# Performance work log

Measured on AMD Instinct MI355X. Metric: run time of the kernel, lower is better.

## Reference

```python
import jax, jax.numpy as jnp
import numpy as np

B, S, H = 4, 1024, 2048
E = 16            # num_experts
K = 2             # num_experts_per_token
I = 1024          # per-expert intermediate_dim
N_SHARED = 2
I_SHARED = I * N_SHARED
RATIO = 0.1       # shared_expert_ratio
EPS = 1e-9


def _swiglu(x, wg, wu, wd):
    # SwiGLU, bias=False: down( silu(gate(x)) * up(x) )
    return (jax.nn.silu(x @ wg) * (x @ wu)) @ wd


def setup_inputs() -> dict:
    key = jax.random.key(0)
    ks = jax.random.split(key, 9)
    scale = 0.02
    x = jax.random.normal(ks[0], (B, S, H), dtype=jnp.float32)
    centroids = jax.random.normal(ks[1], (E, H), dtype=jnp.float32)  # nn.Parameter(randn)
    gate_bias = jnp.zeros((E,), dtype=jnp.float32)
    # shared expert SwiGLU weights (intermediate = I * n_shared_experts)
    wg_s = jax.random.normal(ks[2], (H, I_SHARED), dtype=jnp.float32) * scale
    wu_s = jax.random.normal(ks[3], (H, I_SHARED), dtype=jnp.float32) * scale
    wd_s = jax.random.normal(ks[4], (I_SHARED, H), dtype=jnp.float32) * scale
    # routed experts, stacked [E, ...]
    wg = jax.random.normal(ks[5], (E, H, I), dtype=jnp.float32) * scale
    wu = jax.random.normal(ks[6], (E, H, I), dtype=jnp.float32) * scale
    wd = jax.random.normal(ks[7], (E, I, H), dtype=jnp.float32) * scale
    return {"x": x, "centroids": centroids, "gate_bias": gate_bias,
            "wg_s": wg_s, "wu_s": wu_s, "wd_s": wd_s,
            "wg": wg, "wu": wu, "wd": wd}


def reference(x, centroids, gate_bias, wg_s, wu_s, wd_s, wg, wu, wd):
    # 1) shared expert on ALL tokens, scaled by ratio
    shared = _swiglu(x, wg_s, wu_s, wd_s) * RATIO          # [B,S,H]
    # 2) centroid affinity (DeepSeek-V3 sigmoid gating)
    affinity = jax.nn.sigmoid(jnp.einsum('bsh,eh->bse', x, centroids))  # [B,S,E]
    # 3) bias used ONLY for selection
    biased = affinity + gate_bias
    _, top_idx = jax.lax.top_k(biased, K)                  # [B,S,K]
    # 4) clean weights from unbiased affinity, normalized to sum 1
    top_aff = jnp.take_along_axis(affinity, top_idx, axis=-1)  # [B,S,K]
    weights = top_aff / (top_aff.sum(-1, keepdims=True) + EPS)
    # 5) combine-mask: per-token per-expert weight (0 if not selected)
    mask = (jax.nn.one_hot(top_idx, E, dtype=x.dtype) * weights[..., None]).sum(-2)  # [B,S,E]
    # 6) expert compute + weighted combine; loop over fixed small E avoids
    #    materializing a [B,S,E,H] tensor
    routed = jnp.zeros_like(x)
    for e in range(E):
        routed = routed + mask[..., e:e + 1] * _swiglu(x, wg[e], wu[e], wd[e])
    return shared + routed
```

## Files before the change

kernel.cpp:

```cpp
#include <hip/hip_runtime.h>
#include <hip/hip_bf16.h>

typedef unsigned short u16;
typedef unsigned int u32;
typedef unsigned long long u64;
typedef __attribute__((ext_vector_type(8))) short short8;
typedef __attribute__((ext_vector_type(4))) float f32x4;

#define TOKENS 4096
#define HDIM 2048
#define NEXP 16
#define IDIM 1024
#define ISH 2048
#define MAXT128 80
#define MAXT256 48
#define NCHUNK 128

#define AS1(p) ((const __attribute__((address_space(1))) u32*)(p))
#define AS3(p) ((__attribute__((address_space(3))) u32*)(p))

__device__ __forceinline__ u16 f2b(float f) {
    u32 u = __float_as_uint(f);
    u32 r = u + 0x7fffu + ((u >> 16) & 1u);
    return (u16)(r >> 16);
}

__global__ __launch_bounds__(256) void convert_x_kernel(const float* __restrict__ x,
                                                        u16* __restrict__ xb) {
    size_t i = ((size_t)blockIdx.x * 256 + threadIdx.x) * 8;
    float4 a = *(const float4*)(x + i);
    float4 b = *(const float4*)(x + i + 4);
    u32 p0 = (u32)f2b(a.x) | ((u32)f2b(a.y) << 16);
    u32 p1 = (u32)f2b(a.z) | ((u32)f2b(a.w) << 16);
    u32 p2 = (u32)f2b(b.x) | ((u32)f2b(b.y) << 16);
    u32 p3 = (u32)f2b(b.z) | ((u32)f2b(b.w) << 16);
    uint4 o = make_uint4(p0, p1, p2, p3);
    *(uint4*)(xb + i) = o;
}

__global__ __launch_bounds__(256) void route_kernel(const float* __restrict__ x,
                                                    const float* __restrict__ cent,
                                                    const float* __restrict__ bias,
                                                    int* __restrict__ top_e,
                                                    float* __restrict__ top_w) {
    __shared__ alignas(16) float cs[8 * 2048];
    int lane = threadIdx.x & 63;
    int wv = threadIdx.x >> 6;
    int t = blockIdx.x * 4 + wv;
    const float4* xp4 = (const float4*)(x + (size_t)t * HDIM);
    float4 xr[8];
#pragma unroll
    for (int i = 0; i < 8; i++) xr[i] = xp4[lane + 64 * i];
    float aff[16];
#pragma unroll
    for (int ph = 0; ph < 2; ph++) {
        if (ph) __syncthreads();
        const float* sbase = cent + (size_t)(ph * 8 + wv * 2) * HDIM;
        float* dbase = cs + (size_t)wv * 2 * HDIM;
#pragma unroll
        for (int i = 0; i < 16; i++) {
            __builtin_amdgcn_global_load_lds(AS1(sbase + i * 256 + lane * 4),
                                             AS3(dbase + i * 256), 16, 0, 0);
        }
        __syncthreads();
#pragma unroll
        for (int e = 0; e < 8; e++) {
            const float4* cp = (const float4*)cs + (size_t)e * 512;
            float s = 0.f;
#pragma unroll
            for (int i = 0; i < 8; i++) {
                float4 cv = cp[lane + 64 * i];
                s += xr[i].x * cv.x;
                s += xr[i].y * cv.y;
                s += xr[i].z * cv.z;
                s += xr[i].w * cv.w;
            }
#pragma unroll
            for (int off = 32; off > 0; off >>= 1) s += __shfl_xor(s, off, 64);
            aff[ph * 8 + e] = 1.f / (1.f + expf(-s));
        }
    }
    float b0 = -1e30f, b1 = -1e30f, a0 = 0.f, a1 = 0.f;
    int e0 = -1, e1 = -1;
#pragma unroll
    for (int e = 0; e < 16; e++) {
        float v = aff[e] + bias[e];
        if (v > b0) {
            b1 = b0; e1 = e0; a1 = a0;
            b0 = v; e0 = e; a0 = aff[e];
        } else if (v > b1) {
            b1 = v; e1 = e; a1 = aff[e];
        }
    }
    float inv = 1.f / (a0 + a1 + 1e-9f);
    if (lane == 0) {
        top_e[2 * t] = e0; top_w[2 * t] = a0 * inv;
        top_e[2 * t + 1] = e1; top_w[2 * t + 1] = a1 * inv;
    }
}

__global__ __launch_bounds__(1024) void build_kernel(
    const int* __restrict__ top_e, const float* __restrict__ top_w,
    int* __restrict__ counts, int* __restrict__ offsets,
    int* __restrict__ ntilesA, int* __restrict__ tileA_e, int* __restrict__ tileA_m,
    int* __restrict__ ntilesB, int* __restrict__ tileB_e, int* __restrict__ tileB_m,
    int* __restrict__ list_tok, float* __restrict__ list_w,
    int* __restrict__ tok2slot) {
    __shared__ int cnt[NCHUNK][16];
    __shared__ int offs_s[16];
    __shared__ int totals[16];
    int tid = threadIdx.x;
    int lane = tid & 63, wv = tid >> 6;
    for (int c = wv; c < NCHUNK; c += 16) {
        int v = top_e[c * 64 + lane];
#pragma unroll
        for (int e = 0; e < 16; e++) {
            u64 m = __ballot(v == e);
            if (lane == 0) cnt[c][e] = (int)__popcll(m);
        }
    }
    __syncthreads();
    if (tid < 16) {
        int s = 0;
        for (int c = 0; c < NCHUNK; c++) s += cnt[c][tid];
        totals[tid] = s;
        counts[tid] = s;
    }
    __syncthreads();
    if (tid == 0) {
        int r = 0, ntA = 0, ntB = 0;
        for (int e = 0; e < 16; e++) {
            offs_s[e] = r;
            offsets[e] = r;
            int ce = totals[e];
            int tA = (ce + 127) >> 7;
            for (int m = 0; m < tA; m++) { tileA_e[ntA] = e; tileA_m[ntA] = m; ntA++; }
            int tB = (ce + 255) >> 8;
            for (int m = 0; m < tB; m++) { tileB_e[ntB] = e; tileB_m[ntB] = m; ntB++; }
            r += ce;
        }
        *ntilesA = ntA;
        *ntilesB = ntB;
    }
    __syncthreads();
    if (tid < 16) {
        int r = offs_s[tid];
        for (int c = 0; c < NCHUNK; c++) {
            int v = cnt[c][tid];
            cnt[c][tid] = r;
            r += v;
        }
    }
    __syncthreads();
    for (int c = wv; c < NCHUNK; c += 16) {
        int i = c * 64 + lane;
        int v = top_e[i];
        int rank = 0;
#pragma unroll
        for (int e = 0; e < 16; e++) {
            u64 m = __ballot(v == e);
            if (v == e) rank = (int)__popcll(m & ((1ull << lane) - 1ull));
        }
        int slot = cnt[c][v] + rank;
        list_tok[slot] = i >> 1;
        list_w[slot] = top_w[i];
        tok2slot[i] = slot;
    }
}

__global__ __launch_bounds__(256) void conv_w_kernel(const float* __restrict__ W,
                                                     u16* __restrict__ Wt, int K, int N) {
    int nt = blockIdx.x, kc = blockIdx.y;
    size_t mato = (size_t)blockIdx.z * K * N;
    const float* Wm = W + mato;
    u16* Wtm = Wt + mato;
    int ksB = K >> 5;
    __shared__ u16 Ls[64 * 40];
    int t = threadIdx.x;
    int kr = t >> 3, ng = t & 7;
    int nn = t >> 2, seg = t & 3;
    int g = seg ^ ((nn >> 2) & 3);
#pragma unroll
    for (int s = 0; s < 8; s++) {
        int kb = kc * 256 + s * 32;
        const float* src = Wm + (size_t)(kb + kr) * N + nt * 64 + ng * 8;
        float4 f0 = *(const float4*)src;
        float4 f1 = *(const float4*)(src + 4);
        __syncthreads();
        const float* p0 = (const float*)&f0;
        const float* p1 = (const float*)&f1;
#pragma unroll
        for (int l = 0; l < 4; l++) Ls[(8 * ng + l) * 40 + kr] = f2b(p0[l]);
#pragma unroll
        for (int l = 0; l < 4; l++) Ls[(8 * ng + 4 + l) * 40 + kr] = f2b(p1[l]);
        __syncthreads();
        const u16* lp = &Ls[nn * 40 + g * 8];
        u32 w0 = (u32)lp[0] | ((u32)lp[1] << 16);
        u32 w1 = (u32)lp[2] | ((u32)lp[3] << 16);
        u32 w2 = (u32)lp[4] | ((u32)lp[5] << 16);
        u32 w3 = (u32)lp[6] | ((u32)lp[7] << 16);
        uint4 o = make_uint4(w0, w1, w2, w3);
        *(uint4*)(Wtm + (size_t)(nt * ksB + (kb >> 5)) * 2048 + t * 8) = o;
    }
}

__global__ __launch_bounds__(256) void gemm_gateup(
    const u16* __restrict__ A, const u16* __restrict__ BgAll, const u16* __restrict__ BuAll,
    u16* __restrict__ hout, int Kd, int Nout, const int* __restrict__ counts,
    const int* __restrict__ offsets, const int* __restrict__ ntiles,
    const int* __restrict__ tile_e, const int* __restrict__ tile_m,
    const int* __restrict__ list_tok, int routed) {
    int cnt = TOKENS, base = 0, m0;
    const u16* Bg = BgAll;
    const u16* Bu = BuAll;
    if (routed) {
        int ti = blockIdx.x;
        if (ti >= *ntiles) return;
        int e = tile_e[ti];
        m0 = tile_m[ti] * 128;
        cnt = counts[e];
        base = offsets[e];
        size_t off = (size_t)e * Kd * Nout;
        Bg += off; Bu += off;
    } else {
        m0 = blockIdx.x * 128;
    }
    int ksB = Kd >> 5;
    __shared__ alignas(16) u16 As[128 * 32];
    __shared__ alignas(16) u16 Bgs[64 * 32];
    __shared__ alignas(16) u16 Bus[64 * 32];
    int tid = threadIdx.x;
    int lane = tid & 63, wv = tid >> 6;
    int quad = lane >> 4, mr = lane & 15;
    int n0 = blockIdx.y * 64;
    int gk = (tid & 3) ^ ((tid >> 4) & 3);
    int mg0 = min(m0 + (tid >> 2), cnt - 1);
    int mg1 = min(m0 + 64 + (tid >> 2), cnt - 1);
    size_t sr0 = routed ? (size_t)list_tok[base + mg0] : (size_t)mg0;
    size_t sr1 = routed ? (size_t)list_tok[base + mg1] : (size_t)mg1;
    const u16* ap0 = A + sr0 * Kd + gk * 8;
    const u16* ap1 = A + sr1 * Kd + gk * 8;
    const u16* bgp = Bg + (size_t)blockIdx.y * ksB * 2048 + tid * 8;
    const u16* bup = Bu + (size_t)blockIdx.y * ksB * 2048 + tid * 8;
    u16* AsW = As + wv * 512;
    u16* AsW2 = As + 2048 + wv * 512;
    u16* BgsW = Bgs + wv * 512;
    u16* BusW = Bus + wv * 512;
    int xq = quad ^ ((mr >> 2) & 3);
    const short8* a0p = (const short8*)(As + ((32 * wv + mr) * 4 + xq) * 8);
    const short8* a1p = (const short8*)(As + ((32 * wv + 16 + mr) * 4 + xq) * 8);
    f32x4 accg[2][4], accu[2][4];
#pragma unroll
    for (int i = 0; i < 2; i++)
#pragma unroll
        for (int j = 0; j < 4; j++) { accg[i][j] = (f32x4)0.f; accu[i][j] = (f32x4)0.f; }

    for (int ks = 0; ks < ksB; ks++) {
        __syncthreads();
        __builtin_amdgcn_global_load_lds(AS1(ap0), AS3(AsW), 16, 0, 0);
        __builtin_amdgcn_global_load_lds(AS1(ap1), AS3(AsW2), 16, 0, 0);
        __builtin_amdgcn_global_load_lds(AS1(bgp), AS3(BgsW), 16, 0, 0);
        __builtin_amdgcn_global_load_lds(AS1(bup), AS3(BusW), 16, 0, 0);
        ap0 += 32; ap1 += 32; bgp += 2048; bup += 2048;
        __syncthreads();
        short8 a0 = *a0p;
        short8 a1 = *a1p;
#pragma unroll
        for (int j = 0; j < 4; j++) {
            short8 bg = *(const short8*)(Bgs + (64 * j + mr * 4 + xq) * 8);
            short8 bu = *(const short8*)(Bus + (64 * j + mr * 4 + xq) * 8);
            accg[0][j] = __builtin_amdgcn_mfma_f32_16x16x32_bf16(a0, bg, accg[0][j], 0, 0, 0);
            accg[1][j] = __builtin_amdgcn_mfma_f32_16x16x32_bf16(a1, bg, accg[1][j], 0, 0, 0);
            accu[0][j] = __builtin_amdgcn_mfma_f32_16x16x32_bf16(a0, bu, accu[0][j], 0, 0, 0);
            accu[1][j] = __builtin_amdgcn_mfma_f32_16x16x32_bf16(a1, bu, accu[1][j], 0, 0, 0);
        }
    }
#pragma unroll
    for (int i = 0; i < 2; i++)
#pragma unroll
        for (int j = 0; j < 4; j++)
#pragma unroll
            for (int r = 0; r < 4; r++) {
                int m = m0 + 32 * wv + 16 * i + quad * 4 + r;
                if (m < cnt) {
                    float gv = accg[i][j][r], uv = accu[i][j][r];
                    float h = gv / (1.f + expf(-gv)) * uv;
                    int n = n0 + 16 * j + mr;
                    hout[(size_t)(base + m) * Nout + n] = f2b(h);
                }
            }
}

__global__ __launch_bounds__(256) void gemm_down(
    const u16* __restrict__ A, const u16* __restrict__ BAll, float* __restrict__ outp,
    int Kd, const int* __restrict__ counts, const int* __restrict__ offsets,
    const int* __restrict__ ntiles, const int* __restrict__ tile_e,
    const int* __restrict__ tile_m, const int* __restrict__ list_tok, int routed) {
    int cnt = TOKENS, base = 0, m0;
    const u16* B = BAll;
    if (routed) {
        int ti = blockIdx.x;
        if (ti >= *ntiles) return;
        int e = tile_e[ti];
        m0 = tile_m[ti] * 256;
        cnt = counts[e];
        base = offsets[e];
        B += (size_t)e * Kd * HDIM;
    } else {
        m0 = blockIdx.x * 256;
    }
    int nk = Kd >> 5;
    __shared__ alignas(16) u16 As[2][256 * 32];
    __shared__ alignas(16) u16 Bs[2][64 * 32];
    int tid = threadIdx.x;
    int lane = tid & 63, wv = tid >> 6;
    int quad = lane >> 4, mr = lane & 15;
    int n0 = blockIdx.y * 64;
    int gk = (tid & 3) ^ ((tid >> 4) & 3);
    const u16* ap0;
    const u16* ap1;
    const u16* ap2;
    const u16* ap3;
    {
        int mg0 = base + min(m0 + 0 * 64 + (tid >> 2), cnt - 1);
        int mg1 = base + min(m0 + 1 * 64 + (tid >> 2), cnt - 1);
        int mg2 = base + min(m0 + 2 * 64 + (tid >> 2), cnt - 1);
        int mg3 = base + min(m0 + 3 * 64 + (tid >> 2), cnt - 1);
        ap0 = A + (size_t)mg0 * Kd + gk * 8;
        ap1 = A + (size_t)mg1 * Kd + gk * 8;
        ap2 = A + (size_t)mg2 * Kd + gk * 8;
        ap3 = A + (size_t)mg3 * Kd + gk * 8;
    }
    const u16* bp = B + (size_t)blockIdx.y * nk * 2048 + tid * 8;
    int xq = quad ^ ((mr >> 2) & 3);
    f32x4 acc[4][4];
#pragma unroll
    for (int i = 0; i < 4; i++)
#pragma unroll
        for (int j = 0; j < 4; j++) acc[i][j] = (f32x4)0.f;

#define STAGE_D(b)                                                                        \
    do {                                                                                  \
        __builtin_amdgcn_global_load_lds(AS1(ap0), AS3(&As[b][0 + wv * 512]), 16, 0, 0);  \
        __builtin_amdgcn_global_load_lds(AS1(ap1), AS3(&As[b][2048 + wv * 512]), 16, 0,   \
                                         0);                                              \
        __builtin_amdgcn_global_load_lds(AS1(ap2), AS3(&As[b][4096 + wv * 512]), 16, 0,   \
                                         0);                                              \
        __builtin_amdgcn_global_load_lds(AS1(ap3), AS3(&As[b][6144 + wv * 512]), 16, 0,   \
                                         0);                                              \
        __builtin_amdgcn_global_load_lds(AS1(bp), AS3(&Bs[b][wv * 512]), 16, 0, 0);       \
        ap0 += 32; ap1 += 32; ap2 += 32; ap3 += 32; bp += 2048;                           \
    } while (0)

    STAGE_D(0);
    __syncthreads();
    int cur = 0;
    for (int ks = 0; ks < nk; ks++) {
        if (ks + 1 < nk) STAGE_D(cur ^ 1);
        const u16* Asc = As[cur];
        const u16* Bc = Bs[cur];
        short8 a0 = *(const short8*)(Asc + ((64 * wv + 0 + mr) * 4 + xq) * 8);
        short8 a1 = *(const short8*)(Asc + ((64 * wv + 16 + mr) * 4 + xq) * 8);
        short8 a2 = *(const short8*)(Asc + ((64 * wv + 32 + mr) * 4 + xq) * 8);
        short8 a3 = *(const short8*)(Asc + ((64 * wv + 48 + mr) * 4 + xq) * 8);
#pragma unroll
        for (int j = 0; j < 4; j++) {
            short8 b = *(const short8*)(Bc + ((16 * j + mr) * 4 + xq) * 8);
            acc[0][j] = __builtin_amdgcn_mfma_f32_16x16x32_bf16(a0, b, acc[0][j], 0, 0, 0);
            acc[1][j] = __builtin_amdgcn_mfma_f32_16x16x32_bf16(a1, b, acc[1][j], 0, 0, 0);
            acc[2][j] = __builtin_amdgcn_mfma_f32_16x16x32_bf16(a2, b, acc[2][j], 0, 0, 0);
            acc[3][j] = __builtin_amdgcn_mfma_f32_16x16x32_bf16(a3, b, acc[3][j], 0, 0, 0);
        }
        __syncthreads();
        cur ^= 1;
    }
#undef STAGE_D

#pragma unroll
    for (int i = 0; i < 4; i++)
#pragma unroll
        for (int j = 0; j < 4; j++)
#pragma unroll
            for (int r = 0; r < 4; r++) {
                int m = m0 + 64 * wv + 16 * i + quad * 4 + r;
                if (m >= cnt) continue;
                int n = n0 + 16 * j + mr;
                float v = acc[i][j][r];
                if (routed) {
                    outp[(size_t)(base + m) * HDIM + n] = v;
                } else {
                    outp[(size_t)m * HDIM + n] = 0.1f * v;
                }
            }
}

__global__ __launch_bounds__(256) void combine_kernel(float* __restrict__ out,
                                                      const float* __restrict__ rd,
                                                      const int* __restrict__ tok2slot,
                                                      const float* __restrict__ top_w) {
    int t = blockIdx.x;
    int s0 = tok2slot[2 * t], s1 = tok2slot[2 * t + 1];
    float w0 = top_w[2 * t], w1 = top_w[2 * t + 1];
    const float4* r0 = (const float4*)(rd + (size_t)s0 * HDIM);
    const float4* r1 = (const float4*)(rd + (size_t)s1 * HDIM);
    float4* op = (float4*)(out + (size_t)t * HDIM);
#pragma unroll
    for (int k = 0; k < 2; k++) {
        int c = threadIdx.x + k * 256;
        float4 o = op[c];
        float4 a = r0[c];
        float4 b = r1[c];
        o.x += w0 * a.x + w1 * b.x;
        o.y += w0 * a.y + w1 * b.y;
        o.z += w0 * a.z + w1 * b.z;
        o.w += w0 * a.w + w1 * b.w;
        op[c] = o;
    }
}

extern "C" void kernel_launch(void* const* d_in, const int* in_sizes, int n_in,
                              void* d_out, int out_size, void* d_ws, size_t ws_size,
                              hipStream_t stream) {
    const float* x = (const float*)d_in[0];
    const float* cent = (const float*)d_in[1];
    const float* bias = (const float*)d_in[2];
    const float* wgs = (const float*)d_in[3];
    const float* wus = (const float*)d_in[4];
    const float* wds = (const float*)d_in[5];
    const float* wg = (const float*)d_in[6];
    const float* wu = (const float*)d_in[7];
    const float* wd = (const float*)d_in[8];
    float* out = (float*)d_out;
    char* ws = (char*)d_ws;

    size_t off_wtgs = 0;
    size_t off_wtus = off_wtgs + (size_t)HDIM * ISH * 2;
    size_t off_wtds = off_wtus + (size_t)HDIM * ISH * 2;
    size_t off_wtg = off_wtds + (size_t)ISH * HDIM * 2;
    size_t off_wtu = off_wtg + (size_t)NEXP * HDIM * IDIM * 2;
    size_t off_wtd = off_wtu + (size_t)NEXP * HDIM * IDIM * 2;
    size_t off_xbf = off_wtd + (size_t)NEXP * IDIM * HDIM * 2;
    size_t off_hsh = off_xbf + (size_t)TOKENS * HDIM * 2;
    size_t off_hrt = off_hsh + (size_t)TOKENS * ISH * 2;
    size_t off_meta = off_hrt + (size_t)2 * TOKENS * IDIM * 2;
    size_t need = off_meta + (1 << 20);
    if (ws_size < need) return;

    u16* Wt_gs = (u16*)(ws + off_wtgs);
    u16* Wt_us = (u16*)(ws + off_wtus);
    u16* Wt_ds = (u16*)(ws + off_wtds);
    u16* Wt_g = (u16*)(ws + off_wtg);
    u16* Wt_u = (u16*)(ws + off_wtu);
    u16* Wt_d = (u16*)(ws + off_wtd);
    u16* x_bf = (u16*)(ws + off_xbf);
    u16* h_sh = (u16*)(ws + off_hsh);
    u16* h_rt = (u16*)(ws + off_hrt);
    float* rd = (float*)ws;
    int* counts = (int*)(ws + off_meta);
    int* offsets = counts + 16;
    int* ntilesA = offsets + 16;
    int* ntilesB = ntilesA + 8;
    int* tileA_e = ntilesB + 8;
    int* tileA_m = tileA_e + MAXT128;
    int* tileB_e = tileA_m + MAXT128;
    int* tileB_m = tileB_e + MAXT256;
    int* tok2slot = tileB_m + MAXT256;
    int* top_e = tok2slot + 2 * TOKENS;
    float* top_w = (float*)(top_e + 2 * TOKENS);
    int* list_tok = (int*)(top_w + 2 * TOKENS);
    float* list_w = (float*)(list_tok + 2 * TOKENS);

    convert_x_kernel<<<TOKENS * HDIM / (256 * 8), 256, 0, stream>>>(x, x_bf);
    route_kernel<<<TOKENS / 4, 256, 0, stream>>>(x, cent, bias, top_e, top_w);
    build_kernel<<<1, 1024, 0, stream>>>(top_e, top_w, counts, offsets, ntilesA, tileA_e,
                                         tileA_m, ntilesB, tileB_e, tileB_m, list_tok,
                                         list_w, tok2slot);

    conv_w_kernel<<<dim3(ISH / 64, HDIM / 256, 1), 256, 0, stream>>>(wgs, Wt_gs, HDIM, ISH);
    conv_w_kernel<<<dim3(ISH / 64, HDIM / 256, 1), 256, 0, stream>>>(wus, Wt_us, HDIM, ISH);
    conv_w_kernel<<<dim3(HDIM / 64, ISH / 256, 1), 256, 0, stream>>>(wds, Wt_ds, ISH, HDIM);
    conv_w_kernel<<<dim3(IDIM / 64, HDIM / 256, NEXP), 256, 0, stream>>>(wg, Wt_g, HDIM, IDIM);
    conv_w_kernel<<<dim3(IDIM / 64, HDIM / 256, NEXP), 256, 0, stream>>>(wu, Wt_u, HDIM, IDIM);
    conv_w_kernel<<<dim3(HDIM / 64, IDIM / 256, NEXP), 256, 0, stream>>>(wd, Wt_d, IDIM, HDIM);

    gemm_gateup<<<dim3(TOKENS / 128, ISH / 64, 1), 256, 0, stream>>>(
        x_bf, Wt_gs, Wt_us, h_sh, HDIM, ISH, nullptr, nullptr, nullptr, nullptr, nullptr,
        nullptr, 0);
    gemm_down<<<dim3(TOKENS / 256, HDIM / 64, 1), 256, 0, stream>>>(
        h_sh, Wt_ds, out, ISH, nullptr, nullptr, nullptr, nullptr, nullptr, nullptr, 0);
    gemm_gateup<<<dim3(MAXT128, IDIM / 64, 1), 256, 0, stream>>>(
        x_bf, Wt_g, Wt_u, h_rt, HDIM, IDIM, counts, offsets, ntilesA, tileA_e, tileA_m,
        list_tok, 1);
    gemm_down<<<dim3(MAXT256, HDIM / 64, 1), 256, 0, stream>>>(
        h_rt, Wt_d, rd, IDIM, counts, offsets, ntilesB, tileB_e, tileB_m, list_tok, 1);
    combine_kernel<<<TOKENS, 256, 0, stream>>>(out, rd, tok2slot, top_w);
}
```

Measured before the change: 980.7 us.

## Double K-step per iteration in gate/up and down GEMMs, drop double buffering

Both GEMM kernels now load a K slice of 64 per iteration (two 32-wide sub-tiles) instead of 32, halving the number of barriers and loop iterations. The down GEMM removes its two-stage double-buffered prefetch in favor of a single larger buffer loaded synchronously each iteration. This trades fewer synchronizations and more loads in flight per barrier against losing the overlap of global loads with MFMA compute in the down kernel, and it uses more LDS in the gate/up kernel, which may reduce occupancy.

Result: faster. 884.0 us (-9.9%).

```diff
diff --git a/kernel.cpp b/kernel.cpp
--- a/kernel.cpp
+++ b/kernel.cpp
@@ -225,10 +225,10 @@
     } else {
         m0 = blockIdx.x * 128;
     }
-    int ksB = Kd >> 5;
-    __shared__ alignas(16) u16 As[128 * 32];
-    __shared__ alignas(16) u16 Bgs[64 * 32];
-    __shared__ alignas(16) u16 Bus[64 * 32];
+    int nk = Kd >> 6;
+    __shared__ alignas(16) u16 As[128 * 64];
+    __shared__ alignas(16) u16 Bgs[64 * 64];
+    __shared__ alignas(16) u16 Bus[64 * 64];
     int tid = threadIdx.x;
     int lane = tid & 63, wv = tid >> 6;
     int quad = lane >> 4, mr = lane & 15;
@@ -240,39 +240,41 @@
     size_t sr1 = routed ? (size_t)list_tok[base + mg1] : (size_t)mg1;
     const u16* ap0 = A + sr0 * Kd + gk * 8;
     const u16* ap1 = A + sr1 * Kd + gk * 8;
-    const u16* bgp = Bg + (size_t)blockIdx.y * ksB * 2048 + tid * 8;
-    const u16* bup = Bu + (size_t)blockIdx.y * ksB * 2048 + tid * 8;
-    u16* AsW = As + wv * 512;
-    u16* AsW2 = As + 2048 + wv * 512;
-    u16* BgsW = Bgs + wv * 512;
-    u16* BusW = Bus + wv * 512;
+    size_t bstr = (size_t)(Kd >> 5) * 2048;
+    const u16* bgp = Bg + (size_t)blockIdx.y * bstr + tid * 8;
+    const u16* bup = Bu + (size_t)blockIdx.y * bstr + tid * 8;
     int xq = quad ^ ((mr >> 2) & 3);
-    const short8* a0p = (const short8*)(As + ((32 * wv + mr) * 4 + xq) * 8);
-    const short8* a1p = (const short8*)(As + ((32 * wv + 16 + mr) * 4 + xq) * 8);
     f32x4 accg[2][4], accu[2][4];
 #pragma unroll
     for (int i = 0; i < 2; i++)
 #pragma unroll
         for (int j = 0; j < 4; j++) { accg[i][j] = (f32x4)0.f; accu[i][j] = (f32x4)0.f; }
 
-    for (int ks = 0; ks < ksB; ks++) {
-        __syncthreads();
-        __builtin_amdgcn_global_load_lds(AS1(ap0), AS3(AsW), 16, 0, 0);
-        __builtin_amdgcn_global_load_lds(AS1(ap1), AS3(AsW2), 16, 0, 0);
-        __builtin_amdgcn_global_load_lds(AS1(bgp), AS3(BgsW), 16, 0, 0);
-        __builtin_amdgcn_global_load_lds(AS1(bup), AS3(BusW), 16, 0, 0);
-        ap0 += 32; ap1 += 32; bgp += 2048; bup += 2048;
-        __syncthreads();
-        short8 a0 = *a0p;
-        short8 a1 = *a1p;
-#pragma unroll
-        for (int j = 0; j < 4; j++) {
-            short8 bg = *(const short8*)(Bgs + (64 * j + mr * 4 + xq) * 8);
-            short8 bu = *(const short8*)(Bus + (64 * j + mr * 4 + xq) * 8);
-            accg[0][j] = __builtin_amdgcn_mfma_f32_16x16x32_bf16(a0, bg, accg[0][j], 0, 0, 0);
-            accg[1][j] = __builtin_amdgcn_mfma_f32_16x16x32_bf16(a1, bg, accg[1][j], 0, 0, 0);
-            accu[0][j] = __builtin_amdgcn_mfma_f32_16x16x32_bf16(a0, bu, accu[0][j], 0, 0, 0);
-            accu[1][j] = __builtin_amdgcn_mfma_f32_16x16x32_bf16(a1, bu, accu[1][j], 0, 0, 0);
+    for (int ks = 0; ks < nk; ks++) {
+        __syncthreads();
+        __builtin_amdgcn_global_load_lds(AS1(ap0), AS3(As + wv * 512), 16, 0, 0);
+        __builtin_amdgcn_global_load_lds(AS1(ap0 + 32), AS3(As + 4096 + wv * 512), 16, 0, 0);
+        __builtin_amdgcn_global_load_lds(AS1(ap1), AS3(As + 2048 + wv * 512), 16, 0, 0);
+        __builtin_amdgcn_global_load_lds(AS1(ap1 + 32), AS3(As + 6144 + wv * 512), 16, 0, 0);
+        __builtin_amdgcn_global_load_lds(AS1(bgp), AS3(Bgs + wv * 512), 16, 0, 0);
+        __builtin_amdgcn_global_load_lds(AS1(bgp + 2048), AS3(Bgs + 2048 + wv * 512), 16, 0, 0);
+        __builtin_amdgcn_global_load_lds(AS1(bup), AS3(Bus + wv * 512), 16, 0, 0);
+        __builtin_amdgcn_global_load_lds(AS1(bup + 2048), AS3(Bus + 2048 + wv * 512), 16, 0, 0);
+        ap0 += 64; ap1 += 64; bgp += 4096; bup += 4096;
+        __syncthreads();
+#pragma unroll
+        for (int c = 0; c < 2; c++) {
+            short8 a0 = *(const short8*)(As + c * 4096 + ((32 * wv + mr) * 4 + xq) * 8);
+            short8 a1 = *(const short8*)(As + c * 4096 + ((32 * wv + 16 + mr) * 4 + xq) * 8);
+#pragma unroll
+            for (int j = 0; j < 4; j++) {
+                short8 bg = *(const short8*)(Bgs + c * 2048 + (64 * j + mr * 4 + xq) * 8);
+                short8 bu = *(const short8*)(Bus + c * 2048 + (64 * j + mr * 4 + xq) * 8);
+                accg[0][j] = __builtin_amdgcn_mfma_f32_16x16x32_bf16(a0, bg, accg[0][j], 0, 0, 0);
+                accg[1][j] = __builtin_amdgcn_mfma_f32_16x16x32_bf16(a1, bg, accg[1][j], 0, 0, 0);
+                accu[0][j] = __builtin_amdgcn_mfma_f32_16x16x32_bf16(a0, bu, accu[0][j], 0, 0, 0);
+                accu[1][j] = __builtin_amdgcn_mfma_f32_16x16x32_bf16(a1, bu, accu[1][j], 0, 0, 0);
+            }
         }
     }
 #pragma unroll
@@ -309,9 +311,9 @@
     } else {
         m0 = blockIdx.x * 256;
     }
-    int nk = Kd >> 5;
-    __shared__ alignas(16) u16 As[2][256 * 32];
-    __shared__ alignas(16) u16 Bs[2][64 * 32];
+    int nk = Kd >> 6;
+    __shared__ alignas(16) u16 As[256 * 64];
+    __shared__ alignas(16) u16 Bs[64 * 64];
     int tid = threadIdx.x;
     int lane = tid & 63, wv = tid >> 6;
     int quad = lane >> 4, mr = lane & 15;
@@ -331,7 +333,8 @@
         ap2 = A + (size_t)mg2 * Kd + gk * 8;
         ap3 = A + (size_t)mg3 * Kd + gk * 8;
     }
-    const u16* bp = B + (size_t)blockIdx.y * nk * 2048 + tid * 8;
+    size_t bstr = (size_t)(Kd >> 5) * 2048;
+    const u16* bp = B + (size_t)blockIdx.y * bstr + tid * 8;
     int xq = quad ^ ((mr >> 2) & 3);
     f32x4 acc[4][4];
 #pragma unroll
@@ -339,42 +342,36 @@
 #pragma unroll
         for (int j = 0; j < 4; j++) acc[i][j] = (f32x4)0.f;
 
-#define STAGE_D(b)                                                                        \
-    do {                                                                                  \
-        __builtin_amdgcn_global_load_lds(AS1(ap0), AS3(&As[b][0 + wv * 512]), 16, 0, 0);  \
-        __builtin_amdgcn_global_load_lds(AS1(ap1), AS3(&As[b][2048 + wv * 512]), 16, 0,   \
-                                         0);                                              \
-        __builtin_amdgcn_global_load_lds(AS1(ap2), AS3(&As[b][4096 + wv * 512]), 16, 0,   \
-                                         0);                                              \
-        __builtin_amdgcn_global_load_lds(AS1(ap3), AS3(&As[b][6144 + wv * 512]), 16, 0,   \
-                                         0);                                              \
-        __builtin_amdgcn_global_load_lds(AS1(bp), AS3(&Bs[b][wv * 512]), 16, 0, 0);       \
-        ap0 += 32; ap1 += 32; ap2 += 32; ap3 += 32; bp += 2048;                           \
-    } while (0)
-
-    STAGE_D(0);
-    __syncthreads();
-    int cur = 0;
     for (int ks = 0; ks < nk; ks++) {
-        if (ks + 1 < nk) STAGE_D(cur ^ 1);
-        const u16* Asc = As[cur];
-        const u16* Bc = Bs[cur];
-        short8 a0 = *(const short8*)(Asc + ((64 * wv + 0 + mr) * 4 + xq) * 8);
-        short8 a1 = *(const short8*)(Asc + ((64 * wv + 16 + mr) * 4 + xq) * 8);
-        short8 a2 = *(const short8*)(Asc + ((64 * wv + 32 + mr) * 4 + xq) * 8);
-        short8 a3 = *(const short8*)(Asc + ((64 * wv + 48 + mr) * 4 + xq) * 8);
-#pragma unroll
-        for (int j = 0; j < 4; j++) {
-            short8 b = *(const short8*)(Bc + ((16 * j + mr) * 4 + xq) * 8);
-            acc[0][j] = __builtin_amdgcn_mfma_f32_16x16x32_bf16(a0, b, acc[0][j], 0, 0, 0);
-            acc[1][j] = __builtin_amdgcn_mfma_f32_16x16x32_bf16(a1, b, acc[1][j], 0, 0, 0);
-            acc[2][j] = __builtin_amdgcn_mfma_f32_16x16x32_bf16(a2, b, acc[2][j], 0, 0, 0);
-            acc[3][j] = __builtin_amdgcn_mfma_f32_16x16x32_bf16(a3, b, acc[3][j], 0, 0, 0);
-        }
-        __syncthreads();
-        cur ^= 1;
-    }
-#undef STAGE_D
+        __syncthreads();
+        __builtin_amdgcn_global_load_lds(AS1(ap0), AS3(As + 0 + wv * 512), 16, 0, 0);
+        __builtin_amdgcn_global_load_lds(AS1(ap0 + 32), AS3(As + 8192 + wv * 512), 16, 0, 0);
+        __builtin_amdgcn_global_load_lds(AS1(ap1), AS3(As + 2048 + wv * 512), 16, 0, 0);
+        __builtin_amdgcn_global_load_lds(AS1(ap1 + 32), AS3(As + 10240 + wv * 512), 16, 0, 0);
+        __builtin_amdgcn_global_load_lds(AS1(ap2), AS3(As + 4096 + wv * 512), 16, 0, 0);
+        __builtin_amdgcn_global_load_lds(AS1(ap2 + 32), AS3(As + 12288 + wv * 512), 16, 0, 0);
+        __builtin_amdgcn_global_load_lds(AS1(ap3), AS3(As + 6144 + wv * 512), 16, 0, 0);
+        __builtin_amdgcn_global_load_lds(AS1(ap3 + 32), AS3(As + 14336 + wv * 512), 16, 0, 0);
+        __builtin_amdgcn_global_load_lds(AS1(bp), AS3(Bs + wv * 512), 16, 0, 0);
+        __builtin_amdgcn_global_load_lds(AS1(bp + 2048), AS3(Bs + 2048 + wv * 512), 16, 0, 0);
+        ap0 += 64; ap1 += 64; ap2 += 64; ap3 += 64; bp += 4096;
+        __syncthreads();
+#pragma unroll
+        for (int c = 0; c < 2; c++) {
+            short8 a0 = *(const short8*)(As + c * 8192 + ((64 * wv + 0 + mr) * 4 + xq) * 8);
+            short8 a1 = *(const short8*)(As + c * 8192 + ((64 * wv + 16 + mr) * 4 + xq) * 8);
+            short8 a2 = *(const short8*)(As + c * 8192 + ((64 * wv + 32 + mr) * 4 + xq) * 8);
+            short8 a3 = *(const short8*)(As + c * 8192 + ((64 * wv + 48 + mr) * 4 + xq) * 8);
+#pragma unroll
+            for (int j = 0; j < 4; j++) {
+                short8 b = *(const short8*)(Bs + c * 2048 + (64 * j + mr * 4 + xq) * 8);
+                acc[0][j] = __builtin_amdgcn_mfma_f32_16x16x32_bf16(a0, b, acc[0][j], 0, 0, 0);
+                acc[1][j] = __builtin_amdgcn_mfma_f32_16x16x32_bf16(a1, b, acc[1][j], 0, 0, 0);
+                acc[2][j] = __builtin_amdgcn_mfma_f32_16x16x32_bf16(a2, b, acc[2][j], 0, 0, 0);
+                acc[3][j] = __builtin_amdgcn_mfma_f32_16x16x32_bf16(a3, b, acc[3][j], 0, 0, 0);
+            }
+        }
+    }
 
 #pragma unroll
     for (int i = 0; i < 4; i++)
```
